# Optimization experiments

Hardware: AMD Instinct MI355X
Metric: run time of the kernel (lower is better)

Reference implementation:

```python
import jax, jax.numpy as jnp
import numpy as np

EMBED = 256; NH = 8; NP = 32; STRIDE = 4; FFN = 1024
NUM_IMG = 4; H = 160; W = 160; NOBJ = 2048
HD = EMBED // NH
LN_EPS = 1e-5


def setup_inputs():
    key = jax.random.key(0)
    ks = jax.random.split(key, 16)
    inp = {}
    inp["query"] = jax.random.normal(ks[0], (NOBJ, NH, 1, HD), jnp.float32)
    inp["obj_emb"] = jax.random.normal(ks[1], (NOBJ, EMBED), jnp.float32)
    inp["key_feat"] = jax.random.normal(ks[2], (NUM_IMG, EMBED, H, W), jnp.float32)
    inp["value"] = jax.random.normal(ks[3], (NUM_IMG, EMBED, H, W), jnp.float32)
    ys, xs = jnp.meshgrid(jnp.arange(H, dtype=jnp.float32), jnp.arange(W, dtype=jnp.float32), indexing="ij")
    x2d = jnp.stack([(xs + 0.5) * STRIDE, (ys + 0.5) * STRIDE], axis=0)  # (2,H,W) pixel coords
    inp["img_dense_x2d"] = jnp.broadcast_to(x2d[None], (NUM_IMG, 2, H, W)).astype(jnp.float32)
    inp["img_dense_x2d_mask"] = (jax.random.uniform(ks[4], (NUM_IMG, 1, H, W)) > 0.1).astype(jnp.float32)
    inp["obj_xy_point"] = jax.random.uniform(ks[5], (NOBJ, 2)) * jnp.array([W * STRIDE, H * STRIDE], jnp.float32)
    inp["strides"] = 2.0 ** jax.random.randint(ks[6], (NOBJ,), 2, 5).astype(jnp.float32)  # {4,8,16}
    inp["obj_img_ind"] = jax.random.randint(ks[7], (NOBJ,), 0, NUM_IMG, dtype=jnp.int32)
    s = 1.0 / np.sqrt(EMBED)
    inp["w_off"] = jax.random.uniform(ks[8], (EMBED, NH * NP * 2), minval=-s, maxval=s) * 2.5
    inp["b_off"] = jnp.zeros((NH * NP * 2,), jnp.float32)
    inp["w_out"] = jax.random.uniform(ks[9], (EMBED, EMBED), minval=-s, maxval=s)
    inp["b_out"] = jnp.zeros((EMBED,), jnp.float32)
    inp["ln1_g"] = jnp.ones((EMBED,), jnp.float32)
    inp["ln1_b"] = jnp.zeros((EMBED,), jnp.float32)
    inp["w1"] = jax.random.uniform(ks[10], (EMBED, FFN), minval=-s, maxval=s)
    inp["b1"] = jnp.zeros((FFN,), jnp.float32)
    sf = 1.0 / np.sqrt(FFN)
    inp["w2"] = jax.random.uniform(ks[11], (FFN, EMBED), minval=-sf, maxval=sf)
    inp["b2"] = jnp.zeros((EMBED,), jnp.float32)
    inp["ln2_g"] = jnp.ones((EMBED,), jnp.float32)
    inp["ln2_b"] = jnp.zeros((EMBED,), jnp.float32)
    return inp


def _unnorm(g, size):
    # align_corners=False: pixel index = ((g+1)*size - 1) / 2
    return ((g + 1.0) * size - 1.0) * 0.5


def _bilinear(gather, gx, gy, w_size, h_size, zeros_pad):
    """Bilinear sample. gather(y,x) -> (..., C). border or zeros padding."""
    ix = _unnorm(gx, w_size)
    iy = _unnorm(gy, h_size)
    x0f = jnp.floor(ix); y0f = jnp.floor(iy)
    wx1 = ix - x0f; wy1 = iy - y0f
    x0 = x0f.astype(jnp.int32); y0 = y0f.astype(jnp.int32)
    out = None
    for dx, dy, wgt in ((0, 0, (1 - wx1) * (1 - wy1)), (1, 0, wx1 * (1 - wy1)),
                        (0, 1, (1 - wx1) * wy1), (1, 1, wx1 * wy1)):
        xi = x0 + dx; yi = y0 + dy
        xc = jnp.clip(xi, 0, w_size - 1); yc = jnp.clip(yi, 0, h_size - 1)
        if zeros_pad:
            valid = (xi >= 0) & (xi < w_size) & (yi >= 0) & (yi < h_size)
            wgt = wgt * valid.astype(wgt.dtype)
        term = gather(yc, xc) * wgt[..., None]
        out = term if out is None else out + term
    return out


def _ln(x, g, b):
    m = x.mean(-1, keepdims=True)
    v = jnp.mean(jnp.square(x - m), axis=-1, keepdims=True)
    return (x - m) * jax.lax.rsqrt(v + LN_EPS) * g + b


def _forward(query, obj_emb, key_feat, value, img_dense_x2d, img_dense_x2d_mask,
             obj_xy_point, strides, obj_img_ind,
             w_off, b_off, w_out, b_out, ln1_g, ln1_b, w1, b1, w2, b2, ln2_g, ln2_b):
    N = query.shape[0]
    offsets = (obj_emb @ w_off + b_off).reshape(N, NH, NP, 2)
    loc = obj_xy_point[:, None, None] + offsets * strides[:, None, None, None]  # (N,NH,NP,2)
    gx = loc[..., 0] * (2.0 / (W * STRIDE)) - 1.0
    gy = loc[..., 1] * (2.0 / (H * STRIDE)) - 1.0
    # z grid coordinate lands exactly on slice obj_img_ind (zero depth fraction),
    # so 3D trilinear grid_sample reduces to 2D bilinear on the selected image.
    img = obj_img_ind[:, None, None]          # (N,1,1)
    head = jnp.arange(NH)[None, :, None]      # (1,NH,1)
    key_r = key_feat.reshape(NUM_IMG, NH, HD, H, W)
    val_r = value.reshape(NUM_IMG, NH, HD, H, W)
    k_s = _bilinear(lambda y, x: key_r[img, head, :, y, x], gx, gy, W, H, False)   # (N,NH,NP,HD)
    v_s = _bilinear(lambda y, x: val_r[img, head, :, y, x], gx, gy, W, H, False)   # (N,NH,NP,HD)
    x2d_s = _bilinear(lambda y, x: img_dense_x2d[img, :, y, x], gx, gy, W, H, False)       # (N,NH,NP,2)
    mask_s = _bilinear(lambda y, x: img_dense_x2d_mask[img, :, y, x], gx, gy, W, H, True)  # (N,NH,NP,1)
    q = query[:, :, 0]  # (N,NH,HD)
    a = jnp.einsum('nhd,nhpd->nhp', q, k_s) / np.sqrt(HD)
    a_sm = jax.nn.softmax(a, axis=-1) * mask_s[..., 0]
    out = jnp.einsum('nhpd,nhp->nhd', v_s, a_sm).reshape(N, EMBED)
    out = out @ w_out + b_out + obj_emb
    out = _ln(out, ln1_g, ln1_b)
    out = out + (jax.nn.relu(out @ w1 + b1) @ w2 + b2)
    out = _ln(out, ln2_g, ln2_b)
    v_samples = jnp.swapaxes(v_s, -1, -2)      # (N,NH,HD,NP)
    a_samples = a[:, :, None, :]               # (N,NH,1,NP)
    mask_samples = jnp.swapaxes(mask_s, -1, -2)  # (N,NH,1,NP)
    x2d_samples = jnp.swapaxes(x2d_s, -1, -2)    # (N,NH,2,NP)
    return (out, v_samples, a_samples, mask_samples, x2d_samples)


def reference(query, obj_emb, key_feat, value, img_dense_x2d, img_dense_x2d_mask,
              obj_xy_point, strides, obj_img_ind,
              w_off, b_off, w_out, b_out, ln1_g, ln1_b, w1, b1, w2, b2, ln2_g, ln2_b):
    return _forward(query, obj_emb, key_feat, value, img_dense_x2d, img_dense_x2d_mask,
                    obj_xy_point, strides, obj_img_ind,
                    w_off, b_off, w_out, b_out, ln1_g, ln1_b, w1, b1, w2, b2, ln2_g, ln2_b)
```

## Files before the change

### kernel.cpp

```cpp
#include <hip/hip_runtime.h>
#include <hip/hip_fp16.h>
#include <math.h>

#define NOBJ  2048
#define EMBED 256
#define NHD   8
#define NPT   32
#define HD    32
#define NUMIMG 4
#define HH    160
#define WW    160
#define FFN   1024
#define PLANE (HH*WW)
#define LN_EPS 1e-5f

typedef _Float16 f16x8 __attribute__((ext_vector_type(8)));
typedef float f32x4 __attribute__((ext_vector_type(4)));

__global__ __launch_bounds__(256) void k_offsets(
    const float* __restrict__ obj_emb, const float* __restrict__ w_off,
    const float* __restrict__ b_off, const float* __restrict__ obj_xy,
    const float* __restrict__ strides,
    float* __restrict__ cx, float* __restrict__ cy) {
  const int G = 8;
  __shared__ float s_emb[G][EMBED];
  const int t = threadIdx.x;
  const int n0 = blockIdx.x * G;
  #pragma unroll
  for (int g = 0; g < G; ++g) s_emb[g][t] = obj_emb[(n0 + g) * EMBED + t];
  __syncthreads();

  float ax[G], ay[G];
  #pragma unroll
  for (int g = 0; g < G; ++g) { ax[g] = 0.f; ay[g] = 0.f; }

  const float2* wp = (const float2*)w_off;
  for (int e = 0; e < EMBED; ++e) {
    float2 w = wp[e * 256 + t];
    #pragma unroll
    for (int g = 0; g < G; ++g) {
      float a = s_emb[g][e];
      ax[g] = fmaf(a, w.x, ax[g]);
      ay[g] = fmaf(a, w.y, ay[g]);
    }
  }
  const float bx = b_off[2 * t], by = b_off[2 * t + 1];
  #pragma unroll
  for (int g = 0; g < G; ++g) {
    const int n = n0 + g;
    const float st = strides[n];
    const float lx = obj_xy[2 * n]     + (ax[g] + bx) * st;
    const float ly = obj_xy[2 * n + 1] + (ay[g] + by) * st;
    const float gx = lx * (2.0f / (WW * 4)) - 1.0f;
    const float gy = ly * (2.0f / (HH * 4)) - 1.0f;
    const float ix = ((gx + 1.0f) * WW - 1.0f) * 0.5f;
    const float iy = ((gy + 1.0f) * HH - 1.0f) * 0.5f;
    cx[n * 256 + t] = ix;
    cy[n * 256 + t] = iy;
  }
}

__global__ __launch_bounds__(256) void k_relayout(
    const float* __restrict__ key_feat, const float* __restrict__ value,
    __half* __restrict__ kvh) {
  __shared__ float s[64][33];
  const int t = threadIdx.x;
  const int xt  = blockIdx.x;
  const int y   = blockIdx.y;
  const int img = blockIdx.z;
  const int xl = t & 31, cgrp = t >> 5;
  const int xw = t >> 3, cw = t & 7;

  for (int hh = 0; hh < 8; ++hh) {
    #pragma unroll
    for (int i = 0; i < 8; ++i) {
      const int row = cgrp * 8 + i;
      const float* src = (row & 32) ? value : key_feat;
      const int c = hh * 32 + (row & 31);
      s[row][xl] =
          src[((size_t)(img * 256 + c)) * PLANE + y * WW + xt * 32 + xl];
    }
    __syncthreads();
    __half h8[8];
    #pragma unroll
    for (int j = 0; j < 8; ++j) h8[j] = __float2half(s[cw * 8 + j][xw]);
    const size_t ob = ((size_t)(img * PLANE + y * WW + xt * 32 + xw)) * 512
                      + hh * 64 + cw * 8;
    *(int4*)(kvh + ob) = *(const int4*)h8;
    __syncthreads();
  }
}

__device__ __forceinline__ void acc8(int4 r, float w, float* acc) {
  const __half2* hp = (const __half2*)&r;
  #pragma unroll
  for (int i = 0; i < 4; ++i) {
    const float2 f = __half22float2(hp[i]);
    acc[2 * i]     = fmaf(w, f.x, acc[2 * i]);
    acc[2 * i + 1] = fmaf(w, f.y, acc[2 * i + 1]);
  }
}

__global__ __launch_bounds__(256) void k_sample_hwc(
    const float* __restrict__ query, const __half* __restrict__ kvh,
    const float* __restrict__ x2d, const float* __restrict__ x2d_mask,
    const int* __restrict__ obj_img,
    const float* __restrict__ cx, const float* __restrict__ cy,
    float* __restrict__ o_vs, float* __restrict__ o_as,
    float* __restrict__ o_ms, float* __restrict__ o_x2,
    _Float16* __restrict__ attn_h) {
  __shared__ float s_q[256];
  __shared__ float s_v[NHD * NPT * 33];
  __shared__ float s_asm[256];

  const int n = blockIdx.x;
  const int t = threadIdx.x;
  const int h = t >> 5, p = t & 31;

  s_q[t] = query[n * 256 + t];
  const int img = obj_img[n];
  const float ix = cx[n * 256 + t];
  const float iy = cy[n * 256 + t];

  const float x0f = floorf(ix), y0f = floorf(iy);
  const float wx1 = ix - x0f, wy1 = iy - y0f;
  const int x0 = (int)x0f, y0 = (int)y0f;
  const int x1 = x0 + 1, y1 = y0 + 1;
  const int x0c = min(max(x0, 0), WW - 1), x1c = min(max(x1, 0), WW - 1);
  const int y0c = min(max(y0, 0), HH - 1), y1c = min(max(y1, 0), HH - 1);
  const float w00 = (1.f - wx1) * (1.f - wy1);
  const float w10 = wx1 * (1.f - wy1);
  const float w01 = (1.f - wx1) * wy1;
  const float w11 = wx1 * wy1;
  const int o00 = y0c * WW + x0c, o10 = y0c * WW + x1c;
  const int o01 = y1c * WW + x0c, o11 = y1c * WW + x1c;

  const size_t pb = (size_t)img * PLANE;
  const int4* base = (const int4*)kvh;
  const long b0 = ((long)(pb + o00)) * 64 + h * 8;
  const long b1 = ((long)(pb + o10)) * 64 + h * 8;
  const long b2 = ((long)(pb + o01)) * 64 + h * 8;
  const long b3 = ((long)(pb + o11)) * 64 + h * 8;
  __syncthreads();

  float a_acc = 0.f;
  float* svrow = &s_v[(h * NPT + p) * 33];
  float* vout = o_vs + (size_t)(n * NHD + h) * (HD * NPT) + p;
  #pragma unroll
  for (int ch = 0; ch < 4; ++ch) {
    const int4 k0 = base[b0 + ch],     k1 = base[b1 + ch];
    const int4 k2 = base[b2 + ch],     k3 = base[b3 + ch];
    const int4 v0 = base[b0 + 4 + ch], v1 = base[b1 + 4 + ch];
    const int4 v2 = base[b2 + 4 + ch], v3 = base[b3 + 4 + ch];
    float kc[8] = {0, 0, 0, 0, 0, 0, 0, 0};
    float vc[8] = {0, 0, 0, 0, 0, 0, 0, 0};
    acc8(k0, w00, kc); acc8(k1, w10, kc); acc8(k2, w01, kc); acc8(k3, w11, kc);
    acc8(v0, w00, vc); acc8(v1, w10, vc); acc8(v2, w01, vc); acc8(v3, w11, vc);
    #pragma unroll
    for (int j = 0; j < 8; ++j) {
      const int c = ch * 8 + j;
      a_acc = fmaf(s_q[h * HD + c], kc[j], a_acc);
      svrow[c] = vc[j];
      vout[c * NPT] = vc[j];
    }
  }

  const float a = a_acc * 0.17677669529663687f;
  o_as[n * 256 + t] = a;

  const float* xb0 = x2d + (size_t)img * 2 * PLANE;
  const float* xb1 = xb0 + PLANE;
  const float x2v0 = w00 * xb0[o00] + w10 * xb0[o10] + w01 * xb0[o01] + w11 * xb0[o11];
  const float x2v1 = w00 * xb1[o00] + w10 * xb1[o10] + w01 * xb1[o01] + w11 * xb1[o11];
  o_x2[(size_t)n * 512 + h * 64 + p]      = x2v0;
  o_x2[(size_t)n * 512 + h * 64 + 32 + p] = x2v1;

  const float* mb = x2d_mask + (size_t)img * PLANE;
  const float m00 = (x0 >= 0 && x0 < WW && y0 >= 0 && y0 < HH) ? w00 : 0.f;
  const float m10 = (x1 >= 0 && x1 < WW && y0 >= 0 && y0 < HH) ? w10 : 0.f;
  const float m01 = (x0 >= 0 && x0 < WW && y1 >= 0 && y1 < HH) ? w01 : 0.f;
  const float m11 = (x1 >= 0 && x1 < WW && y1 >= 0 && y1 < HH) ? w11 : 0.f;
  const float m = m00 * mb[o00] + m10 * mb[o10] + m01 * mb[o01] + m11 * mb[o11];
  o_ms[n * 256 + t] = m;

  float mx = a;
  #pragma unroll
  for (int o = 16; o >= 1; o >>= 1) mx = fmaxf(mx, __shfl_xor(mx, o, 32));
  const float ev = expf(a - mx);
  float s = ev;
  #pragma unroll
  for (int o = 16; o >= 1; o >>= 1) s += __shfl_xor(s, o, 32);
  s_asm[t] = ev / s * m;
  __syncthreads();

  const int d = p;
  float o = 0.f;
  const float* svh = &s_v[h * NPT * 33];
  const float* amh = &s_asm[h * NPT];
  #pragma unroll
  for (int pp = 0; pp < NPT; ++pp) o = fmaf(amh[pp], svh[pp * 33 + d], o);
  attn_h[n * 256 + t] = (_Float16)o;
}

__global__ __launch_bounds__(256) void k_cvtw(
    const float* __restrict__ w, _Float16* __restrict__ wT, int K, int N) {
  __shared__ float s[32][33];
  const int t = threadIdx.x;
  const int k0 = blockIdx.x * 32, n0 = blockIdx.y * 32;
  const int nl = t & 31, kg = t >> 5;
  #pragma unroll
  for (int i = 0; i < 4; ++i) {
    const int k = kg * 4 + i;
    s[k][nl] = w[(size_t)(k0 + k) * N + n0 + nl];
  }
  __syncthreads();
  const int kl = t & 31, ng = t >> 5;
  #pragma unroll
  for (int i = 0; i < 4; ++i) {
    const int n = ng * 4 + i;
    wT[(size_t)(n0 + n) * K + k0 + kl] = (_Float16)s[kl][n];
  }
}


__global__ __launch_bounds__(256) void k_gemm_a(
    const _Float16* __restrict__ Ah, const _Float16* __restrict__ BT,
    float* __restrict__ C) {
  const int t = threadIdx.x;
  const int wv = t >> 6, lane = t & 63;
  const int r16 = lane & 15, quad = lane >> 4;
  const int m_base = blockIdx.x * 64 + wv * 16;
  const int n_base = blockIdx.y * 32;
  const _Float16* ap  = Ah + (size_t)(m_base + r16) * 256 + quad * 8;
  const _Float16* bp0 = BT + (size_t)(n_base + r16) * 256 + quad * 8;
  const _Float16* bp1 = bp0 + 16 * 256;
  f32x4 acc0 = {0.f, 0.f, 0.f, 0.f}, acc1 = {0.f, 0.f, 0.f, 0.f};
  #pragma unroll 4
  for (int kc = 0; kc < 256; kc += 32) {
    f16x8 a  = *(const f16x8*)(ap + kc);
    f16x8 b0 = *(const f16x8*)(bp0 + kc);
    f16x8 b1 = *(const f16x8*)(bp1 + kc);
    acc0 = __builtin_amdgcn_mfma_f32_16x16x32_f16(a, b0, acc0, 0, 0, 0);
    acc1 = __builtin_amdgcn_mfma_f32_16x16x32_f16(a, b1, acc1, 0, 0, 0);
  }
  float* cp = C + (size_t)(m_base + quad * 4) * 256 + n_base + r16;
  #pragma unroll
  for (int r = 0; r < 4; ++r) {
    cp[(size_t)r * 256]      = acc0[r];
    cp[(size_t)r * 256 + 16] = acc1[r];
  }
}

__global__ __launch_bounds__(256) void k_gemm_b(
    const _Float16* __restrict__ Ah, const _Float16* __restrict__ BT,
    const float* __restrict__ bias, _Float16* __restrict__ Fh) {
  const int t = threadIdx.x;
  const int wv = t >> 6, lane = t & 63;
  const int r16 = lane & 15, quad = lane >> 4;
  const int m_base = blockIdx.x * 64 + wv * 16;
  const int n_base = blockIdx.y * 32;
  const _Float16* ap  = Ah + (size_t)(m_base + r16) * 256 + quad * 8;
  const _Float16* bp0 = BT + (size_t)(n_base + r16) * 256 + quad * 8;
  const _Float16* bp1 = bp0 + 16 * 256;
  f32x4 acc0 = {0.f, 0.f, 0.f, 0.f}, acc1 = {0.f, 0.f, 0.f, 0.f};
  #pragma unroll 4
  for (int kc = 0; kc < 256; kc += 32) {
    f16x8 a  = *(const f16x8*)(ap + kc);
    f16x8 b0 = *(const f16x8*)(bp0 + kc);
    f16x8 b1 = *(const f16x8*)(bp1 + kc);
    acc0 = __builtin_amdgcn_mfma_f32_16x16x32_f16(a, b0, acc0, 0, 0, 0);
    acc1 = __builtin_amdgcn_mfma_f32_16x16x32_f16(a, b1, acc1, 0, 0, 0);
  }
  const float bb0 = bias[n_base + r16];
  const float bb1 = bias[n_base + 16 + r16];
  _Float16* fp = Fh + (size_t)(m_base + quad * 4) * 1024 + n_base + r16;
  #pragma unroll
  for (int r = 0; r < 4; ++r) {
    fp[(size_t)r * 1024]      = (_Float16)fmaxf(acc0[r] + bb0, 0.f);
    fp[(size_t)r * 1024 + 16] = (_Float16)fmaxf(acc1[r] + bb1, 0.f);
  }
}

__global__ __launch_bounds__(256) void k_gemm_c(
    const _Float16* __restrict__ Ah, const _Float16* __restrict__ BT,
    float* __restrict__ C) {
  const int t = threadIdx.x;
  const int wv = t >> 6, lane = t & 63;
  const int r16 = lane & 15, quad = lane >> 4;
  const int m_base = blockIdx.x * 64 + wv * 16;
  const int n_base = blockIdx.y * 32;
  const _Float16* ap  = Ah + (size_t)(m_base + r16) * 1024 + quad * 8;
  const _Float16* bp0 = BT + (size_t)(n_base + r16) * 1024 + quad * 8;
  const _Float16* bp1 = bp0 + 16 * 1024;
  f32x4 acc0 = {0.f, 0.f, 0.f, 0.f}, acc1 = {0.f, 0.f, 0.f, 0.f};
  #pragma unroll 4
  for (int kc = 0; kc < 1024; kc += 32) {
    f16x8 a  = *(const f16x8*)(ap + kc);
    f16x8 b0 = *(const f16x8*)(bp0 + kc);
    f16x8 b1 = *(const f16x8*)(bp1 + kc);
    acc0 = __builtin_amdgcn_mfma_f32_16x16x32_f16(a, b0, acc0, 0, 0, 0);
    acc1 = __builtin_amdgcn_mfma_f32_16x16x32_f16(a, b1, acc1, 0, 0, 0);
  }
  float* cp = C + (size_t)(m_base + quad * 4) * 256 + n_base + r16;
  #pragma unroll
  for (int r = 0; r < 4; ++r) {
    cp[(size_t)r * 256]      = acc0[r];
    cp[(size_t)r * 256 + 16] = acc1[r];
  }
}

__global__ __launch_bounds__(256) void k_ln1(
    const float* __restrict__ Y1, const float* __restrict__ b_out,
    const float* __restrict__ obj_emb, const float* __restrict__ g,
    const float* __restrict__ b, float* __restrict__ U,
    _Float16* __restrict__ Uh) {
  __shared__ float s_y[8][EMBED + 8];
  const int t = threadIdx.x;
  const int m0 = blockIdx.x * 8;
  const float bo = b_out[t];
  #pragma unroll
  for (int r = 0; r < 8; ++r)
    s_y[r][t] = Y1[(size_t)(m0 + r) * EMBED + t] + bo
                + obj_emb[(size_t)(m0 + r) * EMBED + t];
  __syncthreads();
  const int wv = t >> 6, ln = t & 63;
  #pragma unroll
  for (int k = 0; k < 2; ++k) {
    const int rr = wv * 2 + k;
    const float v0 = s_y[rr][ln], v1 = s_y[rr][ln + 64];
    const float v2 = s_y[rr][ln + 128], v3 = s_y[rr][ln + 192];
    float sum = v0 + v1 + v2 + v3;
    #pragma unroll
    for (int o = 32; o >= 1; o >>= 1) sum += __shfl_xor(sum, o);
    const float mean = sum * (1.0f / EMBED);
    const float d0 = v0 - mean, d1 = v1 - mean, d2 = v2 - mean, d3 = v3 - mean;
    float ss = d0 * d0 + d1 * d1 + d2 * d2 + d3 * d3;
    #pragma unroll
    for (int o = 32; o >= 1; o >>= 1) ss += __shfl_xor(ss, o);
    const float rstd = rsqrtf(ss * (1.0f / EMBED) + LN_EPS);
    const size_t base = (size_t)(m0 + rr) * EMBED;
    const float o0 = d0 * rstd * g[ln]       + b[ln];
    const float o1 = d1 * rstd * g[ln + 64]  + b[ln + 64];
    const float o2 = d2 * rstd * g[ln + 128] + b[ln + 128];
    const float o3 = d3 * rstd * g[ln + 192] + b[ln + 192];
    U[base + ln] = o0;         Uh[base + ln] = (_Float16)o0;
    U[base + ln + 64] = o1;    Uh[base + ln + 64] = (_Float16)o1;
    U[base + ln + 128] = o2;   Uh[base + ln + 128] = (_Float16)o2;
    U[base + ln + 192] = o3;   Uh[base + ln + 192] = (_Float16)o3;
  }
}

__global__ __launch_bounds__(256) void k_ln2(
    const float* __restrict__ Y2, const float* __restrict__ b2,
    const float* __restrict__ U, const float* __restrict__ g,
    const float* __restrict__ b, float* __restrict__ out) {
  __shared__ float s_y[8][EMBED + 8];
  const int t = threadIdx.x;
  const int m0 = blockIdx.x * 8;
  const float bb = b2[t];
  #pragma unroll
  for (int r = 0; r < 8; ++r)
    s_y[r][t] = Y2[(size_t)(m0 + r) * EMBED + t] + bb
                + U[(size_t)(m0 + r) * EMBED + t];
  __syncthreads();
  const int wv = t >> 6, ln = t & 63;
  #pragma unroll
  for (int k = 0; k < 2; ++k) {
    const int rr = wv * 2 + k;
    const float v0 = s_y[rr][ln], v1 = s_y[rr][ln + 64];
    const float v2 = s_y[rr][ln + 128], v3 = s_y[rr][ln + 192];
    float sum = v0 + v1 + v2 + v3;
    #pragma unroll
    for (int o = 32; o >= 1; o >>= 1) sum += __shfl_xor(sum, o);
    const float mean = sum * (1.0f / EMBED);
    const float d0 = v0 - mean, d1 = v1 - mean, d2 = v2 - mean, d3 = v3 - mean;
    float ss = d0 * d0 + d1 * d1 + d2 * d2 + d3 * d3;
    #pragma unroll
    for (int o = 32; o >= 1; o >>= 1) ss += __shfl_xor(ss, o);
    const float rstd = rsqrtf(ss * (1.0f / EMBED) + LN_EPS);
    const size_t base = (size_t)(m0 + rr) * EMBED;
    out[base + ln]       = d0 * rstd * g[ln]       + b[ln];
    out[base + ln + 64]  = d1 * rstd * g[ln + 64]  + b[ln + 64];
    out[base + ln + 128] = d2 * rstd * g[ln + 128] + b[ln + 128];
    out[base + ln + 192] = d3 * rstd * g[ln + 192] + b[ln + 192];
  }
}

extern "C" void kernel_launch(void* const* d_in, const int* in_sizes, int n_in,
                              void* d_out, int out_size, void* d_ws, size_t ws_size,
                              hipStream_t stream) {
  const float* query    = (const float*)d_in[0];
  const float* obj_emb  = (const float*)d_in[1];
  const float* key_feat = (const float*)d_in[2];
  const float* value    = (const float*)d_in[3];
  const float* x2d      = (const float*)d_in[4];
  const float* x2d_mask = (const float*)d_in[5];
  const float* obj_xy   = (const float*)d_in[6];
  const float* strides  = (const float*)d_in[7];
  const int*   obj_img  = (const int*)d_in[8];
  const float* w_off    = (const float*)d_in[9];
  const float* b_off    = (const float*)d_in[10];
  const float* w_out    = (const float*)d_in[11];
  const float* b_out    = (const float*)d_in[12];
  const float* ln1_g    = (const float*)d_in[13];
  const float* ln1_b    = (const float*)d_in[14];
  const float* w1       = (const float*)d_in[15];
  const float* b1       = (const float*)d_in[16];
  const float* w2       = (const float*)d_in[17];
  const float* b2       = (const float*)d_in[18];
  const float* ln2_g    = (const float*)d_in[19];
  const float* ln2_b    = (const float*)d_in[20];

  float* out = (float*)d_out;
  float* o_out = out;
  float* o_vs  = out + 524288;
  float* o_as  = out + 524288 + 16777216;
  float* o_ms  = out + 524288 + 16777216 + 524288;
  float* o_x2  = out + 524288 + 16777216 + 1048576;

  char* wsb = (char*)d_ws;
  __half*    kvh    = (__half*)wsb;
  char* B = wsb + 104857600;
  float*     cx     = (float*)(B);
  float*     Y1     = (float*)(B);
  float*     cy     = (float*)(B + 2097152);
  float*     Y2     = (float*)(B + 2097152);
  float*     U      = (float*)(B + 4194304);
  _Float16*  Fh     = (_Float16*)(B + 6291456);
  _Float16*  attn_h = (_Float16*)(B + 10485760);
  _Float16*  Uh     = (_Float16*)(B + 11534336);
  _Float16*  woT    = (_Float16*)(B + 12582912);
  _Float16*  w1T    = (_Float16*)(B + 12582912 + 131072);
  _Float16*  w2T    = (_Float16*)(B + 12582912 + 131072 + 524288);

  k_offsets<<<NOBJ / 8, 256, 0, stream>>>(obj_emb, w_off, b_off, obj_xy,
                                          strides, cx, cy);
  k_relayout<<<dim3(5, HH, NUMIMG), 256, 0, stream>>>(key_feat, value, kvh);
  k_cvtw<<<dim3(8, 8), 256, 0, stream>>>(w_out, woT, 256, 256);
  k_cvtw<<<dim3(8, 32), 256, 0, stream>>>(w1, w1T, 256, 1024);
  k_cvtw<<<dim3(32, 8), 256, 0, stream>>>(w2, w2T, 1024, 256);
  k_sample_hwc<<<NOBJ, 256, 0, stream>>>(query, kvh, x2d, x2d_mask, obj_img,
                                         cx, cy, o_vs, o_as, o_ms, o_x2,
                                         attn_h);
  k_gemm_a<<<dim3(32, 8), 256, 0, stream>>>(attn_h, woT, Y1);
  k_ln1<<<NOBJ / 8, 256, 0, stream>>>(Y1, b_out, obj_emb, ln1_g, ln1_b, U, Uh);
  k_gemm_b<<<dim3(32, 32), 256, 0, stream>>>(Uh, w1T, b1, Fh);
  k_gemm_c<<<dim3(32, 8), 256, 0, stream>>>(Fh, w2T, Y2);
  k_ln2<<<NOBJ / 8, 256, 0, stream>>>(Y2, b2, U, ln2_g, ln2_b, o_out);
}
```

Baseline: 452.5 us.

## Vectorize and double-buffer global loads in CHW-to-HWC fp16 relayout kernel

The key/value relayout kernel now loads float4 per thread instead of scalars, processes two heads (128 channel rows) per pass instead of one, and prefetches the next pass's global loads into registers while the current pass is written to LDS and out. This is meant to raise memory-level parallelism and cut the number of synchronized iterations in the bandwidth-bound transpose. It doubles shared memory use and adds register pressure for the two float4 buffers.

```diff
diff --git a/kernel.cpp b/kernel.cpp
--- a/kernel.cpp
+++ b/kernel.cpp
@@ -63,32 +63,73 @@
 __global__ __launch_bounds__(256) void k_relayout(
     const float* __restrict__ key_feat, const float* __restrict__ value,
     __half* __restrict__ kvh) {
-  __shared__ float s[64][33];
+  __shared__ float s[128][33];
   const int t = threadIdx.x;
   const int xt  = blockIdx.x;
   const int y   = blockIdx.y;
   const int img = blockIdx.z;
-  const int xl = t & 31, cgrp = t >> 5;
-  const int xw = t >> 3, cw = t & 7;
-
-  for (int hh = 0; hh < 8; ++hh) {
-    #pragma unroll
-    for (int i = 0; i < 8; ++i) {
-      const int row = cgrp * 8 + i;
-      const float* src = (row & 32) ? value : key_feat;
-      const int c = hh * 32 + (row & 31);
-      s[row][xl] =
-          src[((size_t)(img * 256 + c)) * PLANE + y * WW + xt * 32 + xl];
+  const int lrow = t >> 3;
+  const int lc4  = t & 7;
+  const int px0  = t >> 4;
+  const int wj   = t & 15;
+
+  const size_t px_base  = (size_t)y * WW + xt * 32;
+  const size_t img_base = (size_t)img * 256 * PLANE;
+
+  float4 ra[4], rb[4];
+
+  #define ISSUE(p, rg)                                                        \
+    {                                                                         \
+      const size_t cb = (size_t)(p) * 64 * PLANE + px_base + lc4 * 4;         \
+      rg[0] = *(const float4*)(key_feat + img_base + cb + (size_t)lrow * PLANE);        \
+      rg[1] = *(const float4*)(key_feat + img_base + cb + (size_t)(32 + lrow) * PLANE); \
+      rg[2] = *(const float4*)(value    + img_base + cb + (size_t)lrow * PLANE);        \
+      rg[3] = *(const float4*)(value    + img_base + cb + (size_t)(32 + lrow) * PLANE); \
+    }
+
+  #define TO_LDS(rg)                                                          \
+    {                                                                         \
+      _Pragma("unroll")                                                       \
+      for (int i = 0; i < 4; ++i) {                                           \
+        const int r = i * 32 + lrow;                                          \
+        s[r][lc4 * 4 + 0] = rg[i].x;                                          \
+        s[r][lc4 * 4 + 1] = rg[i].y;                                          \
+        s[r][lc4 * 4 + 2] = rg[i].z;                                          \
+        s[r][lc4 * 4 + 3] = rg[i].w;                                          \
+      }                                                                       \
+    }
+
+  const int hc = wj >> 3;
+  const int jj = wj & 7;
+  const int rbase = (jj < 4) ? (hc * 32 + jj * 8)
+                             : (64 + hc * 32 + (jj - 4) * 8);
+  const int chunk_off = hc * 64 + ((jj < 4) ? jj * 8 : 32 + (jj - 4) * 8);
+
+  ISSUE(0, ra);
+  #pragma unroll
+  for (int p = 0; p < 4; ++p) {
+    if (p & 1) {
+      if (p < 3) ISSUE(p + 1, ra);
+      TO_LDS(rb);
+    } else {
+      if (p < 3) ISSUE(p + 1, rb);
+      TO_LDS(ra);
     }
     __syncthreads();
-    __half h8[8];
-    #pragma unroll
-    for (int j = 0; j < 8; ++j) h8[j] = __float2half(s[cw * 8 + j][xw]);
-    const size_t ob = ((size_t)(img * PLANE + y * WW + xt * 32 + xw)) * 512
-                      + hh * 64 + cw * 8;
-    *(int4*)(kvh + ob) = *(const int4*)h8;
+    #pragma unroll
+    for (int i = 0; i < 2; ++i) {
+      const int px = i * 16 + px0;
+      __half h8[8];
+      #pragma unroll
+      for (int m = 0; m < 8; ++m) h8[m] = __float2half(s[rbase + m][px]);
+      const size_t ob = ((size_t)img * PLANE + px_base + px) * 512
+                        + p * 128 + chunk_off;
+      *(int4*)(kvh + ob) = *(const int4*)h8;
+    }
     __syncthreads();
   }
+  #undef ISSUE
+  #undef TO_LDS
 }
 
 __device__ __forceinline__ void acc8(int4 r, float w, float* acc) {
```

After: 452.4 us. Within noise of the previous version (-0.0%).

## Restructure key/value relayout into wide tiles with vectorized loads and half LDS

Applied to the files above, without the earlier changes.

The NCHW-to-HWC fp16 relayout kernel now processes 320 pixels by 128 channels (two heads of key and value) per 512-thread block. It uses float4 global loads and converts to half before storing into a padded shared tile. It then writes back 16-byte records, with one barrier per block instead of two per head iteration. The aim is wider, more coalesced transfers and less sync overhead on a bandwidth-bound transpose. The cost is about 92KB of LDS per block, which limits occupancy, and possible bank conflicts on the scattered half-precision LDS writes.

```diff
diff --git a/kernel.cpp b/kernel.cpp
--- a/kernel.cpp
+++ b/kernel.cpp
@@ -60,34 +60,49 @@
   }
 }
 
-__global__ __launch_bounds__(256) void k_relayout(
+__global__ __launch_bounds__(512) void k_relayout(
     const float* __restrict__ key_feat, const float* __restrict__ value,
     __half* __restrict__ kvh) {
-  __shared__ float s[64][33];
-  const int t = threadIdx.x;
-  const int xt  = blockIdx.x;
-  const int y   = blockIdx.y;
+  __shared__ __half s[320][144];
+  const int t = threadIdx.x;
+  const int Y   = blockIdx.x;
+  const int hp  = blockIdx.y;
   const int img = blockIdx.z;
-  const int xl = t & 31, cgrp = t >> 5;
-  const int xw = t >> 3, cw = t & 7;
-
-  for (int hh = 0; hh < 8; ++hh) {
-    #pragma unroll
-    for (int i = 0; i < 8; ++i) {
-      const int row = cgrp * 8 + i;
-      const float* src = (row & 32) ? value : key_feat;
-      const int c = hh * 32 + (row & 31);
-      s[row][xl] =
-          src[((size_t)(img * 256 + c)) * PLANE + y * WW + xt * 32 + xl];
+  const int pl  = t >> 2;
+  const int q   = t & 3;
+
+  const int sub  = pl & 31;
+  const int grp  = pl >> 5;
+  const int head = hp * 2 + (grp >> 1);
+  const int ch   = head * 32 + sub;
+  const float* src = (grp & 1) ? value : key_feat;
+  const float* sp  = src + ((size_t)img * 256 + ch) * PLANE
+                   + (size_t)Y * 320 + q * 80;
+  const int pxq = q * 80;
+
+  #pragma unroll
+  for (int i0 = 0; i0 < 20; i0 += 10) {
+    float4 r[10];
+    #pragma unroll
+    for (int i = 0; i < 10; ++i) r[i] = *(const float4*)(sp + (i0 + i) * 4);
+    #pragma unroll
+    for (int i = 0; i < 10; ++i) {
+      const int px = pxq + (i0 + i) * 4;
+      s[px + 0][pl] = __float2half(r[i].x);
+      s[px + 1][pl] = __float2half(r[i].y);
+      s[px + 2][pl] = __float2half(r[i].z);
+      s[px + 3][pl] = __float2half(r[i].w);
     }
-    __syncthreads();
-    __half h8[8];
-    #pragma unroll
-    for (int j = 0; j < 8; ++j) h8[j] = __float2half(s[cw * 8 + j][xw]);
-    const size_t ob = ((size_t)(img * PLANE + y * WW + xt * 32 + xw)) * 512
-                      + hh * 64 + cw * 8;
-    *(int4*)(kvh + ob) = *(const int4*)h8;
-    __syncthreads();
+  }
+  __syncthreads();
+
+  const size_t rec = (size_t)img * PLANE + (size_t)Y * 320;
+  #pragma unroll
+  for (int it = 0; it < 10; ++it) {
+    const int flat = it * 512 + t;
+    const int px = flat >> 4, j = flat & 15;
+    const int4 v = *(const int4*)&s[px][j * 8];
+    *(int4*)(kvh + (rec + px) * 512 + hp * 128 + j * 8) = v;
   }
 }
 
@@ -435,7 +450,7 @@
 
   k_offsets<<<NOBJ / 8, 256, 0, stream>>>(obj_emb, w_off, b_off, obj_xy,
                                           strides, cx, cy);
-  k_relayout<<<dim3(5, HH, NUMIMG), 256, 0, stream>>>(key_feat, value, kvh);
+  k_relayout<<<dim3(80, 4, NUMIMG), 512, 0, stream>>>(key_feat, value, kvh);
   k_cvtw<<<dim3(8, 8), 256, 0, stream>>>(w_out, woT, 256, 256);
   k_cvtw<<<dim3(8, 32), 256, 0, stream>>>(w1, w1T, 256, 1024);
   k_cvtw<<<dim3(32, 8), 256, 0, stream>>>(w2, w2T, 1024, 256);
```

After: 448.9 us. Within noise of the previous version (-0.8%).
